# Kernel tuning notes

Hardware: AMD Instinct MI355X
Metric: run time of the kernel (lower is better)

The kernel has to match this reference:

```python
import jax, jax.numpy as jnp
import numpy as np

D = 128          # model_dim
R = 4            # num_relations
H = 64           # hidden width from num_neurons=[64, 64]
N = 50000        # num nodes
E = 800000       # num edges (avg degree 16)
NUM_NODE_TYPES = 3
UPDATE_NODE_TYPES = (0, 1)  # static update_node_type_indices
# update_edge_type_indices = range(R) (all relations), closed over statically


def setup_inputs() -> dict:
    key = jax.random.key(0)
    ks = jax.random.split(key, 12)
    s = 0.05
    return dict(
        node_feature=jax.random.normal(ks[0], (N, D), jnp.float32),
        src=jax.random.randint(ks[1], (E,), 0, N, dtype=jnp.int32),
        dst=jax.random.randint(ks[2], (E,), 0, N, dtype=jnp.int32),
        edge_type=jax.random.randint(ks[3], (E,), 0, R, dtype=jnp.int32),
        node_type=jax.random.randint(ks[4], (N,), 0, NUM_NODE_TYPES, dtype=jnp.int32),
        # per-relation MLP params, stacked over relations
        W1=jax.random.normal(ks[5], (R, D, H), jnp.float32) * s,
        b1=jnp.zeros((R, H), jnp.float32),
        W2=jax.random.normal(ks[6], (R, H, H), jnp.float32) * s,
        b2=jnp.zeros((R, H), jnp.float32),
        W3=jax.random.normal(ks[7], (R, H, D), jnp.float32) * s,
        b3=jnp.zeros((R, D), jnp.float32),
        # node updater: (R+1)*D -> H -> H -> D
        Wu1=jax.random.normal(ks[8], (D * (R + 1), H), jnp.float32) * s,
        bu1=jnp.zeros((H,), jnp.float32),
        Wu2=jax.random.normal(ks[9], (H, H), jnp.float32) * s,
        bu2=jnp.zeros((H,), jnp.float32),
        Wu3=jax.random.normal(ks[10], (H, D), jnp.float32) * s,
        bu3=jnp.zeros((D,), jnp.float32),
    )


def _mlp(x, W1, b1, W2, b2, W3, b3):
    # MLP with ReLU hidden layers, linear output (torch MLP(in, out, [64,64]))
    h = jax.nn.relu(x @ W1 + b1)
    h = jax.nn.relu(h @ W2 + b2)
    return h @ W3 + b3


def reference(node_feature, src, dst, edge_type, node_type,
              W1, b1, W2, b2, W3, b3, Wu1, bu1, Wu2, bu2, Wu3, bu3):
    n = node_feature.shape[0]
    sf = node_feature[src]  # [E, D] gather source features once

    # DGL send_and_recv only writes aggregated features to nodes that receive
    # at least one message; others are zero-filled. Track in-degree > 0.
    indeg = jax.ops.segment_sum(jnp.ones(dst.shape, node_feature.dtype), dst,
                                num_segments=n)
    has_in = (indeg > 0).astype(node_feature.dtype)[:, None]

    blocks = [jax.nn.relu(node_feature) * has_in]  # first D-block of enc input
    for i in range(W1.shape[0]):  # static loop over relations
        msg = jax.nn.relu(_mlp(sf, W1[i], b1[i], W2[i], b2[i], W3[i], b3[i]))
        msg = msg * (edge_type == i)[:, None]  # zero msg for other relations
        blocks.append(jax.ops.segment_sum(msg, dst, num_segments=n))
    enc = jnp.concatenate(blocks, axis=-1)  # [N, (R+1)*D]

    upd = _mlp(enc, Wu1, bu1, Wu2, bu2, Wu3, bu3)  # [N, D]
    upd_mask = jnp.zeros(node_type.shape, bool)
    for t in UPDATE_NODE_TYPES:
        upd_mask = upd_mask | (node_type == t)
    return jnp.where(upd_mask[:, None], upd, node_feature)
```

## Files before the change

### kernel.cpp

```cpp
#include <hip/hip_runtime.h>
#include <hip/hip_bf16.h>

#define D 128
#define H 64
#define R 4
#define NT 64
#define LDC 132
#define CAP 64

typedef __attribute__((ext_vector_type(8))) short bf16x8;
typedef __attribute__((ext_vector_type(4))) float f32x4;

#define PREL 56
#define PFRAG 512
#define UBASE (R * PREL)
#define UPREL 40
#define NFRAG (UBASE + UPREL)

__device__ __forceinline__ float4 relu4(float4 v) {
    return make_float4(fmaxf(v.x, 0.f), fmaxf(v.y, 0.f), fmaxf(v.z, 0.f), fmaxf(v.w, 0.f));
}

__device__ __forceinline__ unsigned short f2bf_rne(float x) {
    unsigned u = __float_as_uint(x);
    return (unsigned short)((u + 0x7fffu + ((u >> 16) & 1u)) >> 16);
}

__device__ __forceinline__ void split1(float x, short& hi, short& lo) {
    unsigned u = __float_as_uint(x);
    unsigned hb = u & 0xffff0000u;
    float res = x - __uint_as_float(hb);
    hi = (short)(u >> 16);
    lo = (short)(__float_as_uint(res) >> 16);
}

__device__ __forceinline__ void split8(const float* x8, bf16x8& hi, bf16x8& lo) {
#pragma unroll
    for (int i = 0; i < 8; ++i) {
        short h, l;
        split1(x8[i], h, l);
        hi[i] = h; lo[i] = l;
    }
}

__device__ __forceinline__ void load_split_A(const float* ap, bf16x8& ah, bf16x8& al) {
    float x8[8];
    *(float4*)&x8[0] = *(const float4*)ap;
    *(float4*)&x8[4] = *(const float4*)(ap + 4);
    split8(x8, ah, al);
}

template<int KSTEPS>
__device__ __forceinline__ void split_strip_A(const float* Ws, int lane, bf16x8* ah, bf16x8* al) {
#pragma unroll
    for (int ks = 0; ks < KSTEPS; ++ks)
        load_split_A(Ws + (lane & 15) * LDC + ks * 32 + ((lane >> 4) << 3), ah[ks], al[ks]);
}

__device__ __forceinline__ void gload_lds16(const void* g, void* l) {
    __builtin_amdgcn_global_load_lds(
        (const __attribute__((address_space(1))) void*)g,
        (__attribute__((address_space(3))) void*)l, 16, 0, 0);
}

__device__ __forceinline__ void stage_chunk(const short* __restrict__ srcH,
                                            short* BbH, int w, int lane) {
#pragma unroll
    for (int f = w; f < 8; f += 4)
        gload_lds16(srcH + ((size_t)f << 9) + (lane << 3), BbH + (f << 9));
}

template<int NCH, int KSTEPS>
__device__ __forceinline__ void compute_chunk(const bf16x8* ah, const bf16x8* al,
                                              const short* BbH,
                                              const short* __restrict__ BloG,
                                              int lane, f32x4* acc) {
#pragma unroll
    for (int ks = 0; ks < KSTEPS; ++ks) {
        bf16x8 bh[NCH], bl[NCH];
#pragma unroll
        for (int n = 0; n < NCH; ++n) {
            int f = n * KSTEPS + ks;
            bh[n] = *(const bf16x8*)(BbH + ((f * 64 + lane) << 3));
            bl[n] = *(const bf16x8*)(BloG + (((size_t)f * 64 + lane) << 3));
        }
#pragma unroll
        for (int n = 0; n < NCH; ++n) {
            acc[n] = __builtin_amdgcn_mfma_f32_16x16x32_bf16(ah[ks], bh[n], acc[n], 0, 0, 0);
            acc[n] = __builtin_amdgcn_mfma_f32_16x16x32_bf16(ah[ks], bl[n], acc[n], 0, 0, 0);
            acc[n] = __builtin_amdgcn_mfma_f32_16x16x32_bf16(al[ks], bh[n], acc[n], 0, 0, 0);
        }
    }
}

template<int NT_TILES, int KSTEPS>
__device__ __forceinline__ void mfma_layer(const float* Als, int ld,
                                           const short* __restrict__ Bhi,
                                           const short* __restrict__ Blo,
                                           int lane, f32x4* acc) {
#pragma unroll
    for (int ks = 0; ks < KSTEPS; ++ks) {
        bf16x8 ah, al;
        load_split_A(Als + (lane & 15) * ld + ks * 32 + ((lane >> 4) << 3), ah, al);
        bf16x8 bh[NT_TILES], bl[NT_TILES];
#pragma unroll
        for (int n = 0; n < NT_TILES; ++n) {
            int f = n * KSTEPS + ks;
            bh[n] = *(const bf16x8*)(Bhi + (((size_t)f * 64 + lane) << 3));
            bl[n] = *(const bf16x8*)(Blo + (((size_t)f * 64 + lane) << 3));
        }
#pragma unroll
        for (int n = 0; n < NT_TILES; ++n) {
            acc[n] = __builtin_amdgcn_mfma_f32_16x16x32_bf16(ah, bh[n], acc[n], 0, 0, 0);
            acc[n] = __builtin_amdgcn_mfma_f32_16x16x32_bf16(ah, bl[n], acc[n], 0, 0, 0);
            acc[n] = __builtin_amdgcn_mfma_f32_16x16x32_bf16(al, bh[n], acc[n], 0, 0, 0);
        }
    }
}

template<int NT_TILES, int KSTEPS>
__device__ __forceinline__ void mfma_layer_regA(const bf16x8* ah, const bf16x8* al,
                                                const short* __restrict__ Bhi,
                                                const short* __restrict__ Blo,
                                                int lane, f32x4* acc) {
#pragma unroll
    for (int ks = 0; ks < KSTEPS; ++ks) {
        bf16x8 bh[NT_TILES], bl[NT_TILES];
#pragma unroll
        for (int n = 0; n < NT_TILES; ++n) {
            int f = n * KSTEPS + ks;
            bh[n] = *(const bf16x8*)(Bhi + (((size_t)f * 64 + lane) << 3));
            bl[n] = *(const bf16x8*)(Blo + (((size_t)f * 64 + lane) << 3));
        }
#pragma unroll
        for (int n = 0; n < NT_TILES; ++n) {
            acc[n] = __builtin_amdgcn_mfma_f32_16x16x32_bf16(ah[ks], bh[n], acc[n], 0, 0, 0);
            acc[n] = __builtin_amdgcn_mfma_f32_16x16x32_bf16(ah[ks], bl[n], acc[n], 0, 0, 0);
            acc[n] = __builtin_amdgcn_mfma_f32_16x16x32_bf16(al[ks], bh[n], acc[n], 0, 0, 0);
        }
    }
}

template<int NT_TILES>
__device__ __forceinline__ void store_C_lds(const f32x4* acc, const float* __restrict__ bias,
                                            float* Ld, int ld, int lane) {
    int r0 = (lane >> 4) << 2;
#pragma unroll
    for (int n = 0; n < NT_TILES; ++n) {
        int col = n * 16 + (lane & 15);
        float bv = bias[col];
#pragma unroll
        for (int q = 0; q < 4; ++q)
            Ld[(r0 + q) * ld + col] = fmaxf(acc[n][q] + bv, 0.f);
    }
}


__global__ __launch_bounds__(256) void k_wprep(
    const float* __restrict__ W1, const float* __restrict__ W2,
    const float* __restrict__ W3, const float* __restrict__ Wu1,
    const float* __restrict__ Wu2, const float* __restrict__ Wu3,
    short* __restrict__ Phi, short* __restrict__ Plo)
{
    int pair = blockIdx.x;
    const float* src; int KS, NTl, fragbase, ncol;
    if (pair < 16) {
        int r = pair >> 2, mat = pair & 3;
        if (mat == 0)      { src = W1  + (size_t)r * (D * H);       KS = 4; NTl = 4; fragbase = r * PREL + 0;  ncol = 64;  }
        else if (mat == 1) { src = W2  + (size_t)r * (H * H);       KS = 2; NTl = 4; fragbase = r * PREL + 16; ncol = 64;  }
        else if (mat == 2) { src = W3  + (size_t)r * (H * D);       KS = 2; NTl = 8; fragbase = r * PREL + 24; ncol = 128; }
        else               { src = Wu1 + (size_t)(r + 1) * D * H;   KS = 4; NTl = 4; fragbase = r * PREL + 40; ncol = 64;  }
    } else {
        int mat = pair - 16;
        if (mat == 0)      { src = Wu1; KS = 4; NTl = 4; fragbase = UBASE + 0;  ncol = 64;  }
        else if (mat == 1) { src = Wu2; KS = 2; NTl = 4; fragbase = UBASE + 16; ncol = 64;  }
        else               { src = Wu3; KS = 2; NTl = 8; fragbase = UBASE + 24; ncol = 128; }
    }
    int nf = NTl * KS;
    for (int u = threadIdx.x; u < nf * 64; u += 256) {
        int f = u >> 6, lane = u & 63;
        int n = f / KS, ks = f - n * KS;
        int col = n * 16 + (lane & 15);
        int k0 = ks * 32 + ((lane >> 4) << 3);
        size_t dstp = (((size_t)(fragbase + f)) * 64 + (size_t)lane) * 8;
#pragma unroll
        for (int i = 0; i < 8; ++i) {
            short h, l;
            split1(src[(size_t)(k0 + i) * ncol + col], h, l);
            Phi[dstp + i] = h;
            Plo[dstp + i] = l;
        }
    }
}


__global__ __launch_bounds__(256, 3) void k_mlp_fill(
    const float* __restrict__ X,
    const float* __restrict__ b1, const float* __restrict__ b2, const float* __restrict__ b3,
    const short* __restrict__ Phi, const short* __restrict__ Plo,
    unsigned short* __restrict__ U, int N, int tiles,
    const int* __restrict__ src, const int* __restrict__ dst,
    const int* __restrict__ etype, int* __restrict__ cnt,
    int* __restrict__ eidx, int E, int mlpB, int fillB)
{
    __shared__ float Bsh[NT * LDC];
    __shared__ short BbH[2][8 * PFRAG];

    const int tid = threadIdx.x;
    const int bid0 = blockIdx.x;

    int minB = (mlpB < fillB) ? mlpB : fillB;
    int lim = 2 * minB;
    bool isFill;
    int mi;
    if (bid0 < lim) { isFill = (bid0 & 1) != 0; mi = bid0 >> 1; }
    else            { isFill = (fillB > mlpB);  mi = minB + (bid0 - lim); }

    if (isFill) {
        int e = mi * 256 + tid;
        if (e < E) {
            int d = dst[e];
            int p = atomicAdd(&cnt[d], 1);
            if (p < CAP) eidx[(size_t)d * CAP + p] = src[e] * 4 + etype[e];
        }
        return;
    }

    const int lane = tid & 63;
    const int w = tid >> 6;
    const int m16 = w * 16;
    const int r = mi / tiles;
    const int n0 = (mi - r * tiles) * NT;

    const short* PH = Phi + (size_t)(r * PREL) * PFRAG;
    const short* PL = Plo + (size_t)(r * PREL) * PFRAG;
    const float* b1r = b1 + r * H;
    const float* b2r = b2 + r * H;
    const float* b3r = b3 + r * D;

    float* Ws = &Bsh[m16 * LDC];

    stage_chunk(PH,             BbH[0], w, lane);
    stage_chunk(PH + 8 * PFRAG, BbH[1], w, lane);

    bf16x8 ahx[4], alx[4];
    {
        int row = n0 + m16 + (lane & 15);
        const float* xp = X + (size_t)row * D + ((lane >> 4) << 3);
        bool ok = (row < N);
#pragma unroll
        for (int ks = 0; ks < 4; ++ks) {
            float x8[8];
            if (ok) {
                *(float4*)&x8[0] = *(const float4*)(xp + ks * 32);
                *(float4*)&x8[4] = *(const float4*)(xp + ks * 32 + 4);
            } else {
#pragma unroll
                for (int i = 0; i < 8; ++i) x8[i] = 0.f;
            }
            split8(x8, ahx[ks], alx[ks]);
        }
    }
    __syncthreads();

    f32x4 acc[8];
#pragma unroll
    for (int n = 0; n < 4; ++n) acc[n] = (f32x4){0.f, 0.f, 0.f, 0.f};
    compute_chunk<2, 4>(ahx, alx, BbH[0], PL, lane, acc + 0);
    __syncthreads();
    stage_chunk(PH + 16 * PFRAG, BbH[0], w, lane);
    compute_chunk<2, 4>(ahx, alx, BbH[1], PL + 8 * PFRAG, lane, acc + 2);
    store_C_lds<4>(acc, b1r, Ws, LDC, lane);
    __syncthreads();
    stage_chunk(PH + 24 * PFRAG, BbH[1], w, lane);

    bf16x8 a2h[2], a2l[2];
    split_strip_A<2>(Ws, lane, a2h, a2l);
#pragma unroll
    for (int n = 0; n < 4; ++n) acc[n] = (f32x4){0.f, 0.f, 0.f, 0.f};
    compute_chunk<4, 2>(a2h, a2l, BbH[0], PL + 16 * PFRAG, lane, acc);
    store_C_lds<4>(acc, b2r, Ws, LDC, lane);
    __syncthreads();
    stage_chunk(PH + 32 * PFRAG, BbH[0], w, lane);

    bf16x8 a3h[2], a3l[2];
    split_strip_A<2>(Ws, lane, a3h, a3l);
#pragma unroll
    for (int n = 0; n < 8; ++n) acc[n] = (f32x4){0.f, 0.f, 0.f, 0.f};
    compute_chunk<4, 2>(a3h, a3l, BbH[1], PL + 24 * PFRAG, lane, acc + 0);
    __syncthreads();
    stage_chunk(PH + 40 * PFRAG, BbH[1], w, lane);
    compute_chunk<4, 2>(a3h, a3l, BbH[0], PL + 32 * PFRAG, lane, acc + 4);
    store_C_lds<8>(acc, b3r, Ws, LDC, lane);
    __syncthreads();
    stage_chunk(PH + 48 * PFRAG, BbH[0], w, lane);

    bf16x8 auh[4], aul[4];
    split_strip_A<4>(Ws, lane, auh, aul);
    f32x4 accu[4];
#pragma unroll
    for (int n = 0; n < 4; ++n) accu[n] = (f32x4){0.f, 0.f, 0.f, 0.f};
    compute_chunk<2, 4>(auh, aul, BbH[1], PL + 40 * PFRAG, lane, accu + 0);
    __syncthreads();
    compute_chunk<2, 4>(auh, aul, BbH[0], PL + 48 * PFRAG, lane, accu + 2);
    {
        int r0 = (lane >> 4) << 2;
#pragma unroll
        for (int n = 0; n < 4; ++n) {
            int col = n * 16 + (lane & 15);
#pragma unroll
            for (int q = 0; q < 4; ++q) {
                int node = n0 + m16 + r0 + q;
                if (node < N)
                    U[((size_t)node * R + r) * H + col] = f2bf_rne(accu[n][q]);
            }
        }
    }
}


__global__ __launch_bounds__(256) void k_gather(
    const unsigned int* __restrict__ U32,
    const int* __restrict__ cnt, const int* __restrict__ eidx,
    float* __restrict__ S, int N)
{
    const int wid = threadIdx.x >> 6, lane = threadIdx.x & 63;
    const int n = blockIdx.x * 4 + wid;
    if (n >= N) return;
    int g = cnt[n]; if (g > CAP) g = CAP;
    const int* ep = eidx + (size_t)n * CAP;
    const int half = lane >> 5;
    const int c2 = lane & 31;
    float ax = 0.f, ay = 0.f;
    {
        int m = g;
        int v = 0;
        if (lane < m) v = ep[lane];
        for (int j0 = 0; j0 < m; j0 += 16) {
            int lim = m - j0; if (lim > 16) lim = 16;
            unsigned t[8];
#pragma unroll
            for (int p = 0; p < 8; ++p) {
                int vi = __shfl(v, j0 + 2 * p + half);
                bool ok = (2 * p + half) < lim;
                t[p] = ok ? U32[(size_t)vi * 32 + c2] : 0u;
            }
#pragma unroll
            for (int p = 0; p < 8; ++p) {
                ax += __uint_as_float(t[p] << 16);
                ay += __uint_as_float(t[p] & 0xffff0000u);
            }
        }
    }
    ax += __shfl_xor(ax, 32);
    ay += __shfl_xor(ay, 32);
    if (half == 0)
        *(float2*)&S[(size_t)n * H + (c2 << 1)] = make_float2(ax, ay);
}


__global__ __launch_bounds__(256, 4) void k_upd(
    const float* __restrict__ X, const float* __restrict__ S,
    const int* __restrict__ cnt, const int* __restrict__ node_type,
    const short* __restrict__ Phi, const short* __restrict__ Plo,
    const float* __restrict__ bu1, const float* __restrict__ bu2, const float* __restrict__ bu3,
    float* __restrict__ out, int N)
{
    __shared__ float Hsh[NT * LDC];

    const int tid = threadIdx.x;
    const int lane = tid & 63;
    const int w = tid >> 6;
    const int m16 = w * 16;
    const int n0 = blockIdx.x * NT;

    const short* PH = Phi + (size_t)UBASE * PFRAG;
    const short* PL = Plo + (size_t)UBASE * PFRAG;

    float* Ws = &Hsh[m16 * LDC];

    bf16x8 ahx[4], alx[4];
    {
        int row = n0 + m16 + (lane & 15);
        bool ok = (row < N) && (cnt[row] > 0);
        const float* xp = X + (size_t)row * D + ((lane >> 4) << 3);
#pragma unroll
        for (int ks = 0; ks < 4; ++ks) {
            float x8[8];
            if (ok) {
                float4 a = *(const float4*)(xp + ks * 32);
                float4 b = *(const float4*)(xp + ks * 32 + 4);
                a = relu4(a); b = relu4(b);
                *(float4*)&x8[0] = a;
                *(float4*)&x8[4] = b;
            } else {
#pragma unroll
                for (int i = 0; i < 8; ++i) x8[i] = 0.f;
            }
            split8(x8, ahx[ks], alx[ks]);
        }
    }

    f32x4 acc[8];
#pragma unroll
    for (int n = 0; n < 4; ++n) acc[n] = (f32x4){0.f, 0.f, 0.f, 0.f};
    mfma_layer_regA<4, 4>(ahx, alx, PH, PL, lane, acc);
    {
        int r0 = (lane >> 4) << 2;
#pragma unroll
        for (int n = 0; n < 4; ++n) {
            int col = n * 16 + (lane & 15);
            float bv = bu1[col];
#pragma unroll
            for (int q = 0; q < 4; ++q) {
                int node = n0 + m16 + r0 + q;
                float sv = (node < N) ? S[(size_t)node * H + col] : 0.f;
                Ws[(r0 + q) * LDC + col] = fmaxf(acc[n][q] + bv + sv, 0.f);
            }
        }
    }

#pragma unroll
    for (int n = 0; n < 4; ++n) acc[n] = (f32x4){0.f, 0.f, 0.f, 0.f};
    mfma_layer<4, 2>(Ws, LDC, PH + (size_t)16 * PFRAG, PL + (size_t)16 * PFRAG, lane, acc);
    store_C_lds<4>(acc, bu2, Ws, LDC, lane);

#pragma unroll
    for (int n = 0; n < 8; ++n) acc[n] = (f32x4){0.f, 0.f, 0.f, 0.f};
    mfma_layer<8, 2>(Ws, LDC, PH + (size_t)24 * PFRAG, PL + (size_t)24 * PFRAG, lane, acc);
    {
        int r0 = (lane >> 4) << 2;
#pragma unroll
        for (int q = 0; q < 4; ++q) {
            int node = n0 + m16 + r0 + q;
            if (node >= N) continue;
            int t = node_type[node];
#pragma unroll
            for (int n = 0; n < 8; ++n) {
                int col = n * 16 + (lane & 15);
                float o = (t <= 1) ? (acc[n][q] + bu3[col])
                                   : X[(size_t)node * D + col];
                out[(size_t)node * D + col] = o;
            }
        }
    }
}

extern "C" void kernel_launch(void* const* d_in, const int* in_sizes, int n_in,
                              void* d_out, int out_size, void* d_ws, size_t ws_size,
                              hipStream_t stream) {
    const float* X     = (const float*)d_in[0];
    const int*   src   = (const int*)d_in[1];
    const int*   dst   = (const int*)d_in[2];
    const int*   etype = (const int*)d_in[3];
    const int*   ntype = (const int*)d_in[4];
    const float* W1    = (const float*)d_in[5];
    const float* b1    = (const float*)d_in[6];
    const float* W2    = (const float*)d_in[7];
    const float* b2    = (const float*)d_in[8];
    const float* W3    = (const float*)d_in[9];
    const float* b3    = (const float*)d_in[10];
    const float* Wu1   = (const float*)d_in[11];
    const float* bu1   = (const float*)d_in[12];
    const float* Wu2   = (const float*)d_in[13];
    const float* bu2   = (const float*)d_in[14];
    const float* Wu3   = (const float*)d_in[15];
    const float* bu3   = (const float*)d_in[16];
    float* out = (float*)d_out;

    const int N = in_sizes[4];
    const int E = in_sizes[1];

    unsigned short* U = (unsigned short*)d_ws;
    float* S    = (float*)(U + (size_t)N * R * H);
    int* cnt    = (int*)(S + (size_t)N * H);
    int* eidx   = cnt + N;
    short* Phi  = (short*)(eidx + (size_t)N * CAP);
    short* Plo  = Phi + (size_t)NFRAG * PFRAG;

    hipMemsetAsync(cnt, 0, (size_t)N * sizeof(int), stream);

    k_wprep<<<19, 256, 0, stream>>>(W1, W2, W3, Wu1, Wu2, Wu3, Phi, Plo);

    int tiles = (N + NT - 1) / NT;
    int mlpB = tiles * R;
    int fillB = (E + 255) / 256;
    k_mlp_fill<<<mlpB + fillB, 256, 0, stream>>>(X, b1, b2, b3, Phi, Plo, U, N, tiles,
                                                 src, dst, etype, cnt, eidx, E, mlpB, fillB);
    k_gather<<<(N + 3) / 4, 256, 0, stream>>>((const unsigned int*)U, cnt, eidx, S, N);
    k_upd<<<tiles, 256, 0, stream>>>(X, S, cnt, ntype, Phi, Plo, bu1, bu2, bu3, out, N);
}
```

Measured before the change: 164.6 us.

## Fold edge-bucketing fill into extra waves of each MLP block

Instead of interleaving separate fill blocks with MLP blocks, each MLP block now launches with 384 threads. The two extra waves bucket a contiguous slice of edges by destination with atomics while the first four waves run the per-relation MLP tile. The fill waves issue a fixed count of barriers so they match the MLP waves' __syncthreads calls. This removes the separate fill-block launches and overlaps the atomic scatter with MFMA work inside each CU. The cost is a larger block, which may reduce occupancy under the launch bounds, and the code only stays correct if the MLP path really uses exactly seven barriers.

```diff
diff --git a/kernel.cpp b/kernel.cpp
--- a/kernel.cpp
+++ b/kernel.cpp
@@ -194,43 +194,40 @@
 }
 
 
-__global__ __launch_bounds__(256, 3) void k_mlp_fill(
+__global__ __launch_bounds__(384, 3) void k_mlp_fill(
     const float* __restrict__ X,
     const float* __restrict__ b1, const float* __restrict__ b2, const float* __restrict__ b3,
     const short* __restrict__ Phi, const short* __restrict__ Plo,
     unsigned short* __restrict__ U, int N, int tiles,
     const int* __restrict__ src, const int* __restrict__ dst,
     const int* __restrict__ etype, int* __restrict__ cnt,
-    int* __restrict__ eidx, int E, int mlpB, int fillB)
+    int* __restrict__ eidx, int E, int epb)
 {
     __shared__ float Bsh[NT * LDC];
     __shared__ short BbH[2][8 * PFRAG];
 
     const int tid = threadIdx.x;
-    const int bid0 = blockIdx.x;
-
-    int minB = (mlpB < fillB) ? mlpB : fillB;
-    int lim = 2 * minB;
-    bool isFill;
-    int mi;
-    if (bid0 < lim) { isFill = (bid0 & 1) != 0; mi = bid0 >> 1; }
-    else            { isFill = (fillB > mlpB);  mi = minB + (bid0 - lim); }
-
-    if (isFill) {
-        int e = mi * 256 + tid;
-        if (e < E) {
+    const int w = tid >> 6;
+    const int bid = blockIdx.x;
+
+    if (w >= 4) {
+        int ftid = tid - 256;
+        int base = bid * epb;
+        int end = base + epb; if (end > E) end = E;
+        for (int e = base + ftid; e < end; e += 128) {
             int d = dst[e];
             int p = atomicAdd(&cnt[d], 1);
             if (p < CAP) eidx[(size_t)d * CAP + p] = src[e] * 4 + etype[e];
         }
+#pragma unroll
+        for (int b = 0; b < 7; ++b) __syncthreads();
         return;
     }
 
     const int lane = tid & 63;
-    const int w = tid >> 6;
     const int m16 = w * 16;
-    const int r = mi / tiles;
-    const int n0 = (mi - r * tiles) * NT;
+    const int r = bid / tiles;
+    const int n0 = (bid - r * tiles) * NT;
 
     const short* PH = Phi + (size_t)(r * PREL) * PFRAG;
     const short* PL = Plo + (size_t)(r * PREL) * PFRAG;
@@ -484,9 +481,9 @@
 
     int tiles = (N + NT - 1) / NT;
     int mlpB = tiles * R;
-    int fillB = (E + 255) / 256;
-    k_mlp_fill<<<mlpB + fillB, 256, 0, stream>>>(X, b1, b2, b3, Phi, Plo, U, N, tiles,
-                                                 src, dst, etype, cnt, eidx, E, mlpB, fillB);
+    int epb = (E + mlpB - 1) / mlpB;
+    k_mlp_fill<<<mlpB, 384, 0, stream>>>(X, b1, b2, b3, Phi, Plo, U, N, tiles,
+                                         src, dst, etype, cnt, eidx, E, epb);
     k_gather<<<(N + 3) / 4, 256, 0, stream>>>((const unsigned int*)U, cnt, eidx, S, N);
     k_upd<<<tiles, 256, 0, stream>>>(X, S, cnt, ntype, Phi, Plo, bu1, bu2, bu3, out, N);
 }
```

New measurement: 159.4 us. 3.2% less time.
